# Optimization experiments

Hardware: AMD Instinct MI355X
Metric: run time of the kernel (lower is better)

## Reference

```python
import jax, jax.numpy as jnp
import numpy as np

EPS = 1e-5
DIM = 1024
HEADS = 8
DIM_HEAD = 64
INNER = HEADS * DIM_HEAD  # 512


def layernorm(x, g, b):
    mu = jnp.mean(x, axis=-1, keepdims=True)
    var = jnp.var(x, axis=-1, keepdims=True)
    return (x - mu) * jax.lax.rsqrt(var + EPS) * g + b


def setup_inputs() -> dict:
    key = jax.random.key(0)
    ks = jax.random.split(key, 5)
    b, t, n, m = 4, 4, 2048, 64
    x = jax.random.normal(ks[0], (b, t, n, DIM), dtype=jnp.float32)
    latents = jax.random.normal(ks[1], (b, t, m, DIM), dtype=jnp.float32)
    Wq = jax.random.normal(ks[2], (DIM, INNER), dtype=jnp.float32) * (DIM ** -0.5)
    Wkv = jax.random.normal(ks[3], (DIM, 2 * INNER), dtype=jnp.float32) * (DIM ** -0.5)
    Wo = jax.random.normal(ks[4], (INNER, DIM), dtype=jnp.float32) * (INNER ** -0.5)
    return {
        "x": x, "latents": latents,
        "g_x": jnp.ones((DIM,), jnp.float32), "b_x": jnp.zeros((DIM,), jnp.float32),
        "g_l": jnp.ones((DIM,), jnp.float32), "b_l": jnp.zeros((DIM,), jnp.float32),
        "Wq": Wq, "Wkv": Wkv, "Wo": Wo,
    }


def reference(x, latents, g_x, b_x, g_l, b_l, Wq, Wkv, Wo):
    b, t, n, d = x.shape
    m = latents.shape[2]
    h, dh = HEADS, DIM_HEAD
    scale = dh ** -0.5

    xn = layernorm(x, g_x, b_x)              # (b,t,n,d)
    ln = layernorm(latents, g_l, b_l)        # (b,t,m,d)

    q = jnp.einsum('btmd,de->btme', ln, Wq)  # (b,t,m,inner)
    kv_in = jnp.concatenate([xn, ln], axis=-2)           # (b,t,n+m,d)
    kv = jnp.einsum('btjd,de->btje', kv_in, Wkv)         # (b,t,n+m,2*inner)
    k, v = jnp.split(kv, 2, axis=-1)

    q = q.reshape(b, t, m, h, dh) * scale
    k = k.reshape(b, t, n + m, h, dh)
    v = v.reshape(b, t, n + m, h, dh)

    sim = jnp.einsum('btihd,btjhd->bhtij', q, k)         # (b,h,t,m,n+m)
    sim = sim - jax.lax.stop_gradient(jnp.max(sim, axis=-1, keepdims=True))
    attn = jax.nn.softmax(sim, axis=-1)
    out = jnp.einsum('bhtij,btjhd->btihd', attn, v)      # (b,t,m,h,dh)
    out = out.reshape(b, t, m, h * dh)
    return jnp.einsum('btme,ed->btmd', out, Wo)          # (b,t,m,d)
```

## Files before the change

### kernel.cpp

```cpp
#include <hip/hip_runtime.h>
#include <cstdint>
#include <cstddef>

typedef __attribute__((ext_vector_type(8))) short short8;
typedef __attribute__((ext_vector_type(4))) short short4v;
typedef __attribute__((ext_vector_type(4))) float f32x4;

__device__ __forceinline__ short f2bf(float f) {
    union { float f; unsigned u; } c; c.f = f;
    unsigned r = c.u + 0x7fffu + ((c.u >> 16) & 1u);
    return (short)(r >> 16);
}

__device__ __forceinline__ void gl2lds16(const void* g, void* l) {
    __builtin_amdgcn_global_load_lds(
        (const __attribute__((address_space(1))) void*)g,
        (__attribute__((address_space(3))) void*)l, 16, 0, 0);
}

__global__ __launch_bounds__(256) void wconv_all(
    const float* __restrict__ Wq, const float* __restrict__ Wkv, const float* __restrict__ Wo,
    short* __restrict__ WqT, short* __restrict__ WkvT, short* __restrict__ WoT)
{
    __shared__ float t[32][33];
    const int id = blockIdx.x;
    const float* S; short* D; int K, N, kt, nt; float scale = 1.0f;
    if (id < 1024)      { S = Wkv; D = WkvT; K = 1024; N = 1024; kt = (id >> 5) * 32;          nt = (id & 31) * 32; }
    else if (id < 1536) { S = Wq;  D = WqT;  K = 1024; N = 512;  kt = ((id - 1024) >> 4) * 32; nt = ((id - 1024) & 15) * 32; scale = 0.125f; }
    else                { S = Wo;  D = WoT;  K = 512;  N = 1024; kt = ((id - 1536) >> 5) * 32; nt = ((id - 1536) & 31) * 32; }
    const int x = threadIdx.x & 31, y4 = (threadIdx.x >> 5) * 4;
    for (int i = 0; i < 4; i++)
        t[y4 + i][x] = S[(size_t)(kt + y4 + i) * N + nt + x];
    __syncthreads();
    for (int i = 0; i < 4; i++)
        D[(size_t)(nt + y4 + i) * K + kt + x] = f2bf(t[x][y4 + i] * scale);
}

__global__ __launch_bounds__(256) void ln_kernel(
    const float* __restrict__ x, const float* __restrict__ lat,
    const float* __restrict__ gx, const float* __restrict__ bx,
    const float* __restrict__ gl, const float* __restrict__ bl,
    short* __restrict__ Aout, short* __restrict__ Lq)
{
    const int wave = threadIdx.x >> 6, lane = threadIdx.x & 63;
    const int r = blockIdx.x * 4 + wave;
    const float *src, *g, *b; size_t drow; short* dst2 = nullptr;
    if (r < 32768) {
        int bt = r >> 11, i = r & 2047;
        src = x + (size_t)r * 1024; g = gx; b = bx;
        drow = (size_t)bt * 2112 + i;
    } else {
        int idx = r - 32768;
        int bt = idx >> 6, i = idx & 63;
        src = lat + (size_t)idx * 1024; g = gl; b = bl;
        drow = (size_t)bt * 2112 + 2048 + i;
        dst2 = Lq + (size_t)idx * 1024;
    }
    float4 v[4];
    for (int j = 0; j < 4; j++) v[j] = ((const float4*)src)[lane + 64 * j];
    float s = 0.f, s2 = 0.f;
    for (int j = 0; j < 4; j++) {
        s  += v[j].x + v[j].y + v[j].z + v[j].w;
        s2 += v[j].x * v[j].x + v[j].y * v[j].y + v[j].z * v[j].z + v[j].w * v[j].w;
    }
    for (int off = 32; off >= 1; off >>= 1) { s += __shfl_xor(s, off); s2 += __shfl_xor(s2, off); }
    const float mu   = s * (1.f / 1024.f);
    const float rstd = rsqrtf(s2 * (1.f / 1024.f) - mu * mu + 1e-5f);
    for (int j = 0; j < 4; j++) {
        float4 gv = ((const float4*)g)[lane + 64 * j];
        float4 bv = ((const float4*)b)[lane + 64 * j];
        short4v o;
        o[0] = f2bf((v[j].x - mu) * rstd * gv.x + bv.x);
        o[1] = f2bf((v[j].y - mu) * rstd * gv.y + bv.y);
        o[2] = f2bf((v[j].z - mu) * rstd * gv.z + bv.z);
        o[3] = f2bf((v[j].w - mu) * rstd * gv.w + bv.w);
        *(short4v*)(Aout + drow * 1024 + (size_t)(lane + 64 * j) * 4) = o;
        if (dst2) *(short4v*)(dst2 + (size_t)(lane + 64 * j) * 4) = o;
    }
}

__global__ __launch_bounds__(256) void gemm_kvq(
    const short* __restrict__ A, const short* __restrict__ Bt, short* __restrict__ C,
    const short* __restrict__ Aq, const short* __restrict__ Btq, short* __restrict__ Cq)
{
    __shared__ short As[128 * 32];
    __shared__ short Bs[128 * 32];
    const int tid  = threadIdx.x;
    const int wave = tid >> 6, lane = tid & 63;
    const int col  = lane & 15, quad = lane >> 4;
    const short *pA, *pB; short* pC; int m0, n0, N;
    if (blockIdx.x < 264) {
        pA = A; pB = Bt; pC = C; N = 1024;
        m0 = blockIdx.x * 128; n0 = blockIdx.y * 128;
    } else {
        int extra = (blockIdx.x - 264) * 8 + blockIdx.y;
        pA = Aq; pB = Btq; pC = Cq; N = 512;
        m0 = (extra >> 2) * 128; n0 = (extra & 3) * 128;
    }
    const int K = 1024;
    const int wm = (wave >> 1) * 64, wn = (wave & 1) * 64;
    const int sr = tid >> 2;
    const int sk = (tid & 3) * 8;

    f32x4 acc[4][4];
    for (int i = 0; i < 4; i++) for (int j = 0; j < 4; j++) acc[i][j] = f32x4{0.f, 0.f, 0.f, 0.f};

    const short* Ar0 = pA + (size_t)(m0 + sr)      * K + sk;
    const short* Ar1 = pA + (size_t)(m0 + sr + 64) * K + sk;
    const short* Br0 = pB + (size_t)(n0 + sr)      * K + sk;
    const short* Br1 = pB + (size_t)(n0 + sr + 64) * K + sk;
    short* lA0 = &As[sr * 32 + sk];
    short* lA1 = &As[(sr + 64) * 32 + sk];
    short* lB0 = &Bs[sr * 32 + sk];
    short* lB1 = &Bs[(sr + 64) * 32 + sk];

    for (int k0 = 0; k0 < K; k0 += 32) {
        __syncthreads();
        gl2lds16(Ar0 + k0, lA0);
        gl2lds16(Ar1 + k0, lA1);
        gl2lds16(Br0 + k0, lB0);
        gl2lds16(Br1 + k0, lB1);
        __syncthreads();
        short8 af[4], bf[4];
        for (int mt = 0; mt < 4; mt++) af[mt] = *(const short8*)&As[(wm + mt * 16 + col) * 32 + quad * 8];
        for (int nt = 0; nt < 4; nt++) bf[nt] = *(const short8*)&Bs[(wn + nt * 16 + col) * 32 + quad * 8];
        for (int mt = 0; mt < 4; mt++)
            for (int nt = 0; nt < 4; nt++)
                acc[mt][nt] = __builtin_amdgcn_mfma_f32_16x16x32_bf16(af[mt], bf[nt], acc[mt][nt], 0, 0, 0);
    }
    for (int mt = 0; mt < 4; mt++)
        for (int nt = 0; nt < 4; nt++)
            for (int r = 0; r < 4; r++) {
                int row = m0 + wm + mt * 16 + quad * 4 + r;
                int cc  = n0 + wn + nt * 16 + col;
                pC[(size_t)row * N + cc] = f2bf(acc[mt][nt][r]);
            }
}

template <typename OutT>
__global__ __launch_bounds__(256) void gemm_bt(
    const short* __restrict__ A, const short* __restrict__ Bt,
    OutT* __restrict__ C, int N, int K)
{
    __shared__ short As[128 * 32];
    __shared__ short Bs[128 * 32];
    const int tid  = threadIdx.x;
    const int wave = tid >> 6, lane = tid & 63;
    const int col  = lane & 15, quad = lane >> 4;
    const int m0 = blockIdx.x * 128, n0 = blockIdx.y * 128;
    const int wm = (wave >> 1) * 64, wn = (wave & 1) * 64;
    const int sr = tid >> 2;
    const int sk = (tid & 3) * 8;

    f32x4 acc[4][4];
    for (int i = 0; i < 4; i++) for (int j = 0; j < 4; j++) acc[i][j] = f32x4{0.f, 0.f, 0.f, 0.f};

    const short* Ar0 = A  + (size_t)(m0 + sr)      * K + sk;
    const short* Ar1 = A  + (size_t)(m0 + sr + 64) * K + sk;
    const short* Br0 = Bt + (size_t)(n0 + sr)      * K + sk;
    const short* Br1 = Bt + (size_t)(n0 + sr + 64) * K + sk;
    short* lA0 = &As[sr * 32 + sk];
    short* lA1 = &As[(sr + 64) * 32 + sk];
    short* lB0 = &Bs[sr * 32 + sk];
    short* lB1 = &Bs[(sr + 64) * 32 + sk];

    for (int k0 = 0; k0 < K; k0 += 32) {
        __syncthreads();
        gl2lds16(Ar0 + k0, lA0);
        gl2lds16(Ar1 + k0, lA1);
        gl2lds16(Br0 + k0, lB0);
        gl2lds16(Br1 + k0, lB1);
        __syncthreads();
        short8 af[4], bf[4];
        for (int mt = 0; mt < 4; mt++) af[mt] = *(const short8*)&As[(wm + mt * 16 + col) * 32 + quad * 8];
        for (int nt = 0; nt < 4; nt++) bf[nt] = *(const short8*)&Bs[(wn + nt * 16 + col) * 32 + quad * 8];
        for (int mt = 0; mt < 4; mt++)
            for (int nt = 0; nt < 4; nt++)
                acc[mt][nt] = __builtin_amdgcn_mfma_f32_16x16x32_bf16(af[mt], bf[nt], acc[mt][nt], 0, 0, 0);
    }
    for (int mt = 0; mt < 4; mt++)
        for (int nt = 0; nt < 4; nt++)
            for (int r = 0; r < 4; r++) {
                int row = m0 + wm + mt * 16 + quad * 4 + r;
                int cc  = n0 + wn + nt * 16 + col;
                float v = acc[mt][nt][r];
                if constexpr (sizeof(OutT) == 2) C[(size_t)row * N + cc] = (OutT)f2bf(v);
                else                             C[(size_t)row * N + cc] = v;
            }
}

__global__ __launch_bounds__(256) void transpose_v(const short* __restrict__ KV, short* __restrict__ Vt)
{
    __shared__ short tile[64 * 68];
    const int bth = blockIdx.y, bt = bth >> 3, h = bth & 7;
    const int jt = blockIdx.x * 64;
    const int tid = threadIdx.x;
    for (int it = 0; it < 2; ++it) {
        int s = tid + it * 256;
        int j = s >> 3, dv = (s & 7) * 8;
        short8 v = *(const short8*)(KV + (size_t)(bt * 2112 + jt + j) * 1024 + 512 + h * 64 + dv);
        short4v lo = {v[0], v[1], v[2], v[3]}, hi = {v[4], v[5], v[6], v[7]};
        *(short4v*)&tile[j * 68 + dv]     = lo;
        *(short4v*)&tile[j * 68 + dv + 4] = hi;
    }
    __syncthreads();
    for (int it = 0; it < 2; ++it) {
        int s = tid + it * 256;
        int d = s >> 3, jv = (s & 7) * 8;
        short8 o;
        for (int jj = 0; jj < 8; jj++) o[jj] = tile[(jv + jj) * 68 + d];
        *(short8*)(Vt + (size_t)(bth * 64 + d) * 2112 + jt + jv) = o;
    }
}

__global__ __launch_bounds__(256) void attn_kernel(
    const short* __restrict__ Q,
    const short* __restrict__ KV,
    const short* __restrict__ Vt,
    float* __restrict__ Opart,
    float* __restrict__ Mp,
    float* __restrict__ Lp)
{
    __shared__ __align__(16) short p_lds[4][64 * 72];
    __shared__ float sm[4][64];
    __shared__ float sl[4][64];
    float* oacc = (float*)&p_lds[0][0];

    const int wg = blockIdx.x;
    const int ck = blockIdx.y;
    const int wgc = wg * 4 + ck;
    const int bt = wg >> 3, h = wg & 7;
    const int tid = threadIdx.x;
    const int wave = tid >> 6, lane = tid & 63;
    const int col = lane & 15, quad = lane >> 4;

    short8 qf[4][2];
    for (int mt = 0; mt < 4; mt++)
        for (int ks = 0; ks < 2; ks++)
            qf[mt][ks] = *(const short8*)(Q + (size_t)(bt * 64 + mt * 16 + col) * 512
                                            + h * 64 + ks * 32 + quad * 8);

    float m_run[4][4], l_run[4][4];
    f32x4 o_acc[4][4];
    for (int mt = 0; mt < 4; mt++)
        for (int r = 0; r < 4; r++) { m_run[mt][r] = -__builtin_inff(); l_run[mt][r] = 0.f; }
    for (int mt = 0; mt < 4; mt++)
        for (int dt = 0; dt < 4; dt++) o_acc[mt][dt] = f32x4{0.f, 0.f, 0.f, 0.f};

    short* pl = p_lds[wave];

    for (int jb = ck * 4 + wave; jb < 33; jb += 16) {
        f32x4 s[4][4];
        for (int mt = 0; mt < 4; mt++) for (int nt = 0; nt < 4; nt++) s[mt][nt] = f32x4{0.f, 0.f, 0.f, 0.f};
        for (int nt = 0; nt < 4; nt++) {
            const int j = jb * 64 + nt * 16 + col;
            const short* kp = KV + (size_t)(bt * 2112 + j) * 1024 + h * 64 + quad * 8;
            short8 k0 = *(const short8*)kp;
            short8 k1 = *(const short8*)(kp + 32);
            for (int mt = 0; mt < 4; mt++) {
                s[mt][nt] = __builtin_amdgcn_mfma_f32_16x16x32_bf16(qf[mt][0], k0, s[mt][nt], 0, 0, 0);
                s[mt][nt] = __builtin_amdgcn_mfma_f32_16x16x32_bf16(qf[mt][1], k1, s[mt][nt], 0, 0, 0);
            }
        }
        for (int mt = 0; mt < 4; mt++)
            for (int r = 0; r < 4; r++) {
                float mx = fmaxf(fmaxf(s[mt][0][r], s[mt][1][r]), fmaxf(s[mt][2][r], s[mt][3][r]));
                for (int off = 8; off >= 1; off >>= 1) mx = fmaxf(mx, __shfl_xor(mx, off));
                float mnew = fmaxf(m_run[mt][r], mx);
                float alpha = __expf(m_run[mt][r] - mnew);
                float rs = 0.f;
                for (int nt = 0; nt < 4; nt++) {
                    float p = __expf(s[mt][nt][r] - mnew);
                    s[mt][nt][r] = p;
                    rs += p;
                }
                for (int off = 8; off >= 1; off >>= 1) rs += __shfl_xor(rs, off);
                m_run[mt][r] = mnew;
                l_run[mt][r] = l_run[mt][r] * alpha + rs;
                for (int dt = 0; dt < 4; dt++) o_acc[mt][dt][r] *= alpha;
            }
        for (int mt = 0; mt < 4; mt++)
            for (int nt = 0; nt < 4; nt++)
                for (int r = 0; r < 4; r++)
                    pl[(mt * 16 + quad * 4 + r) * 72 + nt * 16 + col] = f2bf(s[mt][nt][r]);
        for (int ks = 0; ks < 2; ks++) {
            short8 vf[4];
            for (int dt = 0; dt < 4; dt++)
                vf[dt] = *(const short8*)(Vt + (size_t)(wg * 64 + dt * 16 + col) * 2112
                                             + jb * 64 + ks * 32 + quad * 8);
            for (int mt = 0; mt < 4; mt++) {
                short8 pf = *(const short8*)(pl + (mt * 16 + col) * 72 + ks * 32 + quad * 8);
                for (int dt = 0; dt < 4; dt++)
                    o_acc[mt][dt] = __builtin_amdgcn_mfma_f32_16x16x32_bf16(pf, vf[dt], o_acc[mt][dt], 0, 0, 0);
            }
        }
    }

    if (col == 0)
        for (int mt = 0; mt < 4; mt++)
            for (int r = 0; r < 4; r++) {
                int row = mt * 16 + quad * 4 + r;
                sm[wave][row] = m_run[mt][r];
                sl[wave][row] = l_run[mt][r];
            }
    __syncthreads();
    for (int mt = 0; mt < 4; mt++)
        for (int r = 0; r < 4; r++) {
            int row = mt * 16 + quad * 4 + r;
            float M = fmaxf(fmaxf(sm[0][row], sm[1][row]), fmaxf(sm[2][row], sm[3][row]));
            float L = sl[0][row] * __expf(sm[0][row] - M) + sl[1][row] * __expf(sm[1][row] - M)
                    + sl[2][row] * __expf(sm[2][row] - M) + sl[3][row] * __expf(sm[3][row] - M);
            if (wave == 0 && col == 0) { Mp[wgc * 64 + row] = M; Lp[wgc * 64 + row] = L; }
            float sc = __expf(m_run[mt][r] - M);
            for (int dt = 0; dt < 4; dt++) o_acc[mt][dt][r] *= sc;
        }
    for (int i = tid; i < 64 * 64; i += 256) oacc[i] = 0.f;
    __syncthreads();
    for (int w = 0; w < 4; w++) {
        if (wave == w)
            for (int mt = 0; mt < 4; mt++)
                for (int dt = 0; dt < 4; dt++)
                    for (int r = 0; r < 4; r++)
                        oacc[(mt * 16 + quad * 4 + r) * 64 + dt * 16 + col] += o_acc[mt][dt][r];
        __syncthreads();
    }
    for (int i = tid; i < 64 * 64; i += 256)
        Opart[(size_t)wgc * 4096 + i] = oacc[i];
}

__global__ __launch_bounds__(256) void attn_merge(
    const float* __restrict__ Opart, const float* __restrict__ Mp,
    const float* __restrict__ Lp, short* __restrict__ AttO)
{
    int idx = blockIdx.x * 256 + threadIdx.x;
    int wg = idx >> 12, rd = idx & 4095, row = rd >> 6, d = rd & 63;
    float M = -__builtin_inff();
    for (int c = 0; c < 4; c++) M = fmaxf(M, Mp[(wg * 4 + c) * 64 + row]);
    float L = 0.f, O = 0.f;
    for (int c = 0; c < 4; c++) {
        float e = __expf(Mp[(wg * 4 + c) * 64 + row] - M);
        L += e * Lp[(wg * 4 + c) * 64 + row];
        O += e * Opart[(size_t)(wg * 4 + c) * 4096 + rd];
    }
    int bt = wg >> 3, h = wg & 7;
    AttO[(size_t)(bt * 64 + row) * 512 + h * 64 + d] = f2bf(O / L);
}

extern "C" void kernel_launch(void* const* d_in, const int* in_sizes, int n_in,
                              void* d_out, int out_size, void* d_ws, size_t ws_size,
                              hipStream_t stream)
{
    const float* x   = (const float*)d_in[0];
    const float* lat = (const float*)d_in[1];
    const float* g_x = (const float*)d_in[2];
    const float* b_x = (const float*)d_in[3];
    const float* g_l = (const float*)d_in[4];
    const float* b_l = (const float*)d_in[5];
    const float* Wq  = (const float*)d_in[6];
    const float* Wkv = (const float*)d_in[7];
    const float* Wo  = (const float*)d_in[8];
    float* out = (float*)d_out;

    char* ws = (char*)d_ws;
    size_t off = 0;
    auto alloc = [&](size_t bytes) { char* p = ws + off; off += (bytes + 255) & ~(size_t)255; return p; };
    short* A_kvin = (short*)alloc(33792ull * 1024 * 2);
    short* Lq     = (short*)alloc(1024ull * 1024 * 2);
    short* WkvT   = (short*)alloc(1024ull * 1024 * 2);
    short* WqT    = (short*)alloc(512ull * 1024 * 2);
    short* WoT    = (short*)alloc(1024ull * 512 * 2);
    short* KVb    = (short*)alloc(33792ull * 1024 * 2);
    short* Qb     = (short*)alloc(1024ull * 512 * 2);
    short* AttO   = (short*)alloc(1024ull * 512 * 2);
    short* Vt    = A_kvin;
    char*  sc2   = (char*)A_kvin + 36ull * 1024 * 1024;
    float* Opart = (float*)sc2;
    float* Mp    = (float*)(sc2 + 8388608);
    float* Lp    = (float*)(sc2 + 8388608 + 131072);

    wconv_all<<<2048, 256, 0, stream>>>(Wq, Wkv, Wo, WqT, WkvT, WoT);
    ln_kernel<<<8448, 256, 0, stream>>>(x, lat, g_x, b_x, g_l, b_l, A_kvin, Lq);
    gemm_kvq<<<dim3(268, 8), 256, 0, stream>>>(A_kvin, WkvT, KVb, Lq, WqT, Qb);
    transpose_v<<<dim3(33, 128), 256, 0, stream>>>(KVb, Vt);
    attn_kernel<<<dim3(128, 4), 256, 0, stream>>>(Qb, KVb, Vt, Opart, Mp, Lp);
    attn_merge<<<2048, 256, 0, stream>>>(Opart, Mp, Lp, AttO);
    gemm_bt<float><<<dim3(8, 8), 256, 0, stream>>>(AttO, WoT, out, 1024, 512);
}
```

Before: 388.3 us.

## Fuse V transpose into KV GEMM epilogue, merge prep kernels, deepen K step

The KV projection epilogue now writes K to a separate compact buffer and writes V directly in the transposed per-head layout. This removes the standalone transpose_v kernel and its extra read and write of V. The weight conversion and layernorm kernels are merged into one launch, and both GEMMs now stage 64 of K per barrier pair using two LDS buffers, halving the number of syncs. The risks are the uncoalesced short4 scattered stores in the V epilogue and the larger LDS footprint per block.

```diff
diff --git a/kernel.cpp b/kernel.cpp
--- a/kernel.cpp
+++ b/kernel.cpp
@@ -18,83 +18,83 @@
         (__attribute__((address_space(3))) void*)l, 16, 0, 0);
 }
 
-__global__ __launch_bounds__(256) void wconv_all(
-    const float* __restrict__ Wq, const float* __restrict__ Wkv, const float* __restrict__ Wo,
-    short* __restrict__ WqT, short* __restrict__ WkvT, short* __restrict__ WoT)
-{
-    __shared__ float t[32][33];
-    const int id = blockIdx.x;
-    const float* S; short* D; int K, N, kt, nt; float scale = 1.0f;
-    if (id < 1024)      { S = Wkv; D = WkvT; K = 1024; N = 1024; kt = (id >> 5) * 32;          nt = (id & 31) * 32; }
-    else if (id < 1536) { S = Wq;  D = WqT;  K = 1024; N = 512;  kt = ((id - 1024) >> 4) * 32; nt = ((id - 1024) & 15) * 32; scale = 0.125f; }
-    else                { S = Wo;  D = WoT;  K = 512;  N = 1024; kt = ((id - 1536) >> 5) * 32; nt = ((id - 1536) & 31) * 32; }
-    const int x = threadIdx.x & 31, y4 = (threadIdx.x >> 5) * 4;
-    for (int i = 0; i < 4; i++)
-        t[y4 + i][x] = S[(size_t)(kt + y4 + i) * N + nt + x];
-    __syncthreads();
-    for (int i = 0; i < 4; i++)
-        D[(size_t)(nt + y4 + i) * K + kt + x] = f2bf(t[x][y4 + i] * scale);
-}
-
-__global__ __launch_bounds__(256) void ln_kernel(
+__global__ __launch_bounds__(256) void prep_kernel(
     const float* __restrict__ x, const float* __restrict__ lat,
     const float* __restrict__ gx, const float* __restrict__ bx,
     const float* __restrict__ gl, const float* __restrict__ bl,
-    short* __restrict__ Aout, short* __restrict__ Lq)
-{
-    const int wave = threadIdx.x >> 6, lane = threadIdx.x & 63;
-    const int r = blockIdx.x * 4 + wave;
-    const float *src, *g, *b; size_t drow; short* dst2 = nullptr;
-    if (r < 32768) {
-        int bt = r >> 11, i = r & 2047;
-        src = x + (size_t)r * 1024; g = gx; b = bx;
-        drow = (size_t)bt * 2112 + i;
+    short* __restrict__ Aout, short* __restrict__ Lq,
+    const float* __restrict__ Wq, const float* __restrict__ Wkv, const float* __restrict__ Wo,
+    short* __restrict__ WqT, short* __restrict__ WkvT, short* __restrict__ WoT)
+{
+    __shared__ float t[32][33];
+    if (blockIdx.x < 8448) {
+        const int wave = threadIdx.x >> 6, lane = threadIdx.x & 63;
+        const int r = blockIdx.x * 4 + wave;
+        const float *src, *g, *b; size_t drow; short* dst2 = nullptr;
+        if (r < 32768) {
+            int bt = r >> 11, i = r & 2047;
+            src = x + (size_t)r * 1024; g = gx; b = bx;
+            drow = (size_t)bt * 2112 + i;
+        } else {
+            int idx = r - 32768;
+            int bt = idx >> 6, i = idx & 63;
+            src = lat + (size_t)idx * 1024; g = gl; b = bl;
+            drow = (size_t)bt * 2112 + 2048 + i;
+            dst2 = Lq + (size_t)idx * 1024;
+        }
+        float4 v[4];
+        for (int j = 0; j < 4; j++) v[j] = ((const float4*)src)[lane + 64 * j];
+        float s = 0.f, s2 = 0.f;
+        for (int j = 0; j < 4; j++) {
+            s  += v[j].x + v[j].y + v[j].z + v[j].w;
+            s2 += v[j].x * v[j].x + v[j].y * v[j].y + v[j].z * v[j].z + v[j].w * v[j].w;
+        }
+        for (int off = 32; off >= 1; off >>= 1) { s += __shfl_xor(s, off); s2 += __shfl_xor(s2, off); }
+        const float mu   = s * (1.f / 1024.f);
+        const float rstd = rsqrtf(s2 * (1.f / 1024.f) - mu * mu + 1e-5f);
+        for (int j = 0; j < 4; j++) {
+            float4 gv = ((const float4*)g)[lane + 64 * j];
+            float4 bv = ((const float4*)b)[lane + 64 * j];
+            short4v o;
+            o[0] = f2bf((v[j].x - mu) * rstd * gv.x + bv.x);
+            o[1] = f2bf((v[j].y - mu) * rstd * gv.y + bv.y);
+            o[2] = f2bf((v[j].z - mu) * rstd * gv.z + bv.z);
+            o[3] = f2bf((v[j].w - mu) * rstd * gv.w + bv.w);
+            *(short4v*)(Aout + drow * 1024 + (size_t)(lane + 64 * j) * 4) = o;
+            if (dst2) *(short4v*)(dst2 + (size_t)(lane + 64 * j) * 4) = o;
+        }
     } else {
-        int idx = r - 32768;
-        int bt = idx >> 6, i = idx & 63;
-        src = lat + (size_t)idx * 1024; g = gl; b = bl;
-        drow = (size_t)bt * 2112 + 2048 + i;
-        dst2 = Lq + (size_t)idx * 1024;
-    }
-    float4 v[4];
-    for (int j = 0; j < 4; j++) v[j] = ((const float4*)src)[lane + 64 * j];
-    float s = 0.f, s2 = 0.f;
-    for (int j = 0; j < 4; j++) {
-        s  += v[j].x + v[j].y + v[j].z + v[j].w;
-        s2 += v[j].x * v[j].x + v[j].y * v[j].y + v[j].z * v[j].z + v[j].w * v[j].w;
-    }
-    for (int off = 32; off >= 1; off >>= 1) { s += __shfl_xor(s, off); s2 += __shfl_xor(s2, off); }
-    const float mu   = s * (1.f / 1024.f);
-    const float rstd = rsqrtf(s2 * (1.f / 1024.f) - mu * mu + 1e-5f);
-    for (int j = 0; j < 4; j++) {
-        float4 gv = ((const float4*)g)[lane + 64 * j];
-        float4 bv = ((const float4*)b)[lane + 64 * j];
-        short4v o;
-        o[0] = f2bf((v[j].x - mu) * rstd * gv.x + bv.x);
-        o[1] = f2bf((v[j].y - mu) * rstd * gv.y + bv.y);
-        o[2] = f2bf((v[j].z - mu) * rstd * gv.z + bv.z);
-        o[3] = f2bf((v[j].w - mu) * rstd * gv.w + bv.w);
-        *(short4v*)(Aout + drow * 1024 + (size_t)(lane + 64 * j) * 4) = o;
-        if (dst2) *(short4v*)(dst2 + (size_t)(lane + 64 * j) * 4) = o;
+        const int id = blockIdx.x - 8448;
+        const float* S; short* D; int K, N, kt, nt; float scale = 1.0f;
+        if (id < 1024)      { S = Wkv; D = WkvT; K = 1024; N = 1024; kt = (id >> 5) * 32;          nt = (id & 31) * 32; }
+        else if (id < 1536) { S = Wq;  D = WqT;  K = 1024; N = 512;  kt = ((id - 1024) >> 4) * 32; nt = ((id - 1024) & 15) * 32; scale = 0.125f; }
+        else                { S = Wo;  D = WoT;  K = 512;  N = 1024; kt = ((id - 1536) >> 5) * 32; nt = ((id - 1536) & 31) * 32; }
+        const int xx = threadIdx.x & 31, y4 = (threadIdx.x >> 5) * 4;
+        for (int i = 0; i < 4; i++)
+            t[y4 + i][xx] = S[(size_t)(kt + y4 + i) * N + nt + xx];
+        __syncthreads();
+        for (int i = 0; i < 4; i++)
+            D[(size_t)(nt + y4 + i) * K + kt + xx] = f2bf(t[xx][y4 + i] * scale);
     }
 }
 
 __global__ __launch_bounds__(256) void gemm_kvq(
-    const short* __restrict__ A, const short* __restrict__ Bt, short* __restrict__ C,
-    const short* __restrict__ Aq, const short* __restrict__ Btq, short* __restrict__ Cq)
-{
-    __shared__ short As[128 * 32];
-    __shared__ short Bs[128 * 32];
+    const short* __restrict__ A, const short* __restrict__ Bt,
+    short* __restrict__ Kb, short* __restrict__ Vt,
+    const short* __restrict__ Aq, const short* __restrict__ Btq, short* __restrict__ Qb)
+{
+    __shared__ short As0[128 * 32], As1[128 * 32];
+    __shared__ short Bs0[128 * 32], Bs1[128 * 32];
     const int tid  = threadIdx.x;
     const int wave = tid >> 6, lane = tid & 63;
     const int col  = lane & 15, quad = lane >> 4;
-    const short *pA, *pB; short* pC; int m0, n0, N;
+    const short *pA, *pB; int m0, n0, kvmode;
     if (blockIdx.x < 264) {
-        pA = A; pB = Bt; pC = C; N = 1024;
+        pA = A; pB = Bt; kvmode = 1;
         m0 = blockIdx.x * 128; n0 = blockIdx.y * 128;
     } else {
         int extra = (blockIdx.x - 264) * 8 + blockIdx.y;
-        pA = Aq; pB = Btq; pC = Cq; N = 512;
+        pA = Aq; pB = Btq; kvmode = 0;
         m0 = (extra >> 2) * 128; n0 = (extra & 3) * 128;
     }
     const int K = 1024;
@@ -109,113 +109,123 @@
     const short* Ar1 = pA + (size_t)(m0 + sr + 64) * K + sk;
     const short* Br0 = pB + (size_t)(n0 + sr)      * K + sk;
     const short* Br1 = pB + (size_t)(n0 + sr + 64) * K + sk;
-    short* lA0 = &As[sr * 32 + sk];
-    short* lA1 = &As[(sr + 64) * 32 + sk];
-    short* lB0 = &Bs[sr * 32 + sk];
-    short* lB1 = &Bs[(sr + 64) * 32 + sk];
-
-    for (int k0 = 0; k0 < K; k0 += 32) {
-        __syncthreads();
-        gl2lds16(Ar0 + k0, lA0);
-        gl2lds16(Ar1 + k0, lA1);
-        gl2lds16(Br0 + k0, lB0);
-        gl2lds16(Br1 + k0, lB1);
-        __syncthreads();
-        short8 af[4], bf[4];
-        for (int mt = 0; mt < 4; mt++) af[mt] = *(const short8*)&As[(wm + mt * 16 + col) * 32 + quad * 8];
-        for (int nt = 0; nt < 4; nt++) bf[nt] = *(const short8*)&Bs[(wn + nt * 16 + col) * 32 + quad * 8];
+    short* lA0 = &As0[sr * 32 + sk];  short* lA1 = &As0[(sr + 64) * 32 + sk];
+    short* lA2 = &As1[sr * 32 + sk];  short* lA3 = &As1[(sr + 64) * 32 + sk];
+    short* lB0 = &Bs0[sr * 32 + sk];  short* lB1 = &Bs0[(sr + 64) * 32 + sk];
+    short* lB2 = &Bs1[sr * 32 + sk];  short* lB3 = &Bs1[(sr + 64) * 32 + sk];
+
+    for (int k0 = 0; k0 < K; k0 += 64) {
+        __syncthreads();
+        gl2lds16(Ar0 + k0, lA0);      gl2lds16(Ar1 + k0, lA1);
+        gl2lds16(Ar0 + k0 + 32, lA2); gl2lds16(Ar1 + k0 + 32, lA3);
+        gl2lds16(Br0 + k0, lB0);      gl2lds16(Br1 + k0, lB1);
+        gl2lds16(Br0 + k0 + 32, lB2); gl2lds16(Br1 + k0 + 32, lB3);
+        __syncthreads();
+        {
+            short8 af[4], bf[4];
+            for (int mt = 0; mt < 4; mt++) af[mt] = *(const short8*)&As0[(wm + mt * 16 + col) * 32 + quad * 8];
+            for (int nt = 0; nt < 4; nt++) bf[nt] = *(const short8*)&Bs0[(wn + nt * 16 + col) * 32 + quad * 8];
+            for (int mt = 0; mt < 4; mt++)
+                for (int nt = 0; nt < 4; nt++)
+                    acc[mt][nt] = __builtin_amdgcn_mfma_f32_16x16x32_bf16(af[mt], bf[nt], acc[mt][nt], 0, 0, 0);
+        }
+        {
+            short8 af[4], bf[4];
+            for (int mt = 0; mt < 4; mt++) af[mt] = *(const short8*)&As1[(wm + mt * 16 + col) * 32 + quad * 8];
+            for (int nt = 0; nt < 4; nt++) bf[nt] = *(const short8*)&Bs1[(wn + nt * 16 + col) * 32 + quad * 8];
+            for (int mt = 0; mt < 4; mt++)
+                for (int nt = 0; nt < 4; nt++)
+                    acc[mt][nt] = __builtin_amdgcn_mfma_f32_16x16x32_bf16(af[mt], bf[nt], acc[mt][nt], 0, 0, 0);
+        }
+    }
+    if (kvmode) {
+        for (int mt = 0; mt < 4; mt++)
+            for (int nt = 0; nt < 4; nt++) {
+                int ng = n0 + wn + nt * 16 + col;
+                int base_m = m0 + wm + mt * 16 + quad * 4;
+                if (ng < 512) {
+                    for (int r = 0; r < 4; r++)
+                        Kb[(size_t)(base_m + r) * 512 + ng] = f2bf(acc[mt][nt][r]);
+                } else {
+                    int nv = ng - 512, h = nv >> 6, d = nv & 63;
+                    int bt = base_m / 2112, j = base_m - bt * 2112;
+                    short4v pk;
+                    for (int r = 0; r < 4; r++) pk[r] = f2bf(acc[mt][nt][r]);
+                    *(short4v*)&Vt[(size_t)((bt * 8 + h) * 64 + d) * 2112 + j] = pk;
+                }
+            }
+    } else {
         for (int mt = 0; mt < 4; mt++)
             for (int nt = 0; nt < 4; nt++)
-                acc[mt][nt] = __builtin_amdgcn_mfma_f32_16x16x32_bf16(af[mt], bf[nt], acc[mt][nt], 0, 0, 0);
+                for (int r = 0; r < 4; r++) {
+                    int row = m0 + wm + mt * 16 + quad * 4 + r;
+                    int cc  = n0 + wn + nt * 16 + col;
+                    Qb[(size_t)row * 512 + cc] = f2bf(acc[mt][nt][r]);
+                }
+    }
+}
+
+__global__ __launch_bounds__(256) void gemm_out(
+    const short* __restrict__ A, const short* __restrict__ Bt, float* __restrict__ C)
+{
+    __shared__ short As0[128 * 32], As1[128 * 32];
+    __shared__ short Bs0[128 * 32], Bs1[128 * 32];
+    const int tid  = threadIdx.x;
+    const int wave = tid >> 6, lane = tid & 63;
+    const int col  = lane & 15, quad = lane >> 4;
+    const int m0 = blockIdx.x * 128, n0 = blockIdx.y * 128;
+    const int K = 512, N = 1024;
+    const int wm = (wave >> 1) * 64, wn = (wave & 1) * 64;
+    const int sr = tid >> 2, sk = (tid & 3) * 8;
+
+    f32x4 acc[4][4];
+    for (int i = 0; i < 4; i++) for (int j = 0; j < 4; j++) acc[i][j] = f32x4{0.f, 0.f, 0.f, 0.f};
+
+    const short* Ar0 = A  + (size_t)(m0 + sr)      * K + sk;
+    const short* Ar1 = A  + (size_t)(m0 + sr + 64) * K + sk;
+    const short* Br0 = Bt + (size_t)(n0 + sr)      * K + sk;
+    const short* Br1 = Bt + (size_t)(n0 + sr + 64) * K + sk;
+    short* lA0 = &As0[sr * 32 + sk];  short* lA1 = &As0[(sr + 64) * 32 + sk];
+    short* lA2 = &As1[sr * 32 + sk];  short* lA3 = &As1[(sr + 64) * 32 + sk];
+    short* lB0 = &Bs0[sr * 32 + sk];  short* lB1 = &Bs0[(sr + 64) * 32 + sk];
+    short* lB2 = &Bs1[sr * 32 + sk];  short* lB3 = &Bs1[(sr + 64) * 32 + sk];
+
+    for (int k0 = 0; k0 < K; k0 += 64) {
+        __syncthreads();
+        gl2lds16(Ar0 + k0, lA0);      gl2lds16(Ar1 + k0, lA1);
+        gl2lds16(Ar0 + k0 + 32, lA2); gl2lds16(Ar1 + k0 + 32, lA3);
+        gl2lds16(Br0 + k0, lB0);      gl2lds16(Br1 + k0, lB1);
+        gl2lds16(Br0 + k0 + 32, lB2); gl2lds16(Br1 + k0 + 32, lB3);
+        __syncthreads();
+        {
+            short8 af[4], bf[4];
+            for (int mt = 0; mt < 4; mt++) af[mt] = *(const short8*)&As0[(wm + mt * 16 + col) * 32 + quad * 8];
+            for (int nt = 0; nt < 4; nt++) bf[nt] = *(const short8*)&Bs0[(wn + nt * 16 + col) * 32 + quad * 8];
+            for (int mt = 0; mt < 4; mt++)
+                for (int nt = 0; nt < 4; nt++)
+                    acc[mt][nt] = __builtin_amdgcn_mfma_f32_16x16x32_bf16(af[mt], bf[nt], acc[mt][nt], 0, 0, 0);
+        }
+        {
+            short8 af[4], bf[4];
+            for (int mt = 0; mt < 4; mt++) af[mt] = *(const short8*)&As1[(wm + mt * 16 + col) * 32 + quad * 8];
+            for (int nt = 0; nt < 4; nt++) bf[nt] = *(const short8*)&Bs1[(wn + nt * 16 + col) * 32 + quad * 8];
+            for (int mt = 0; mt < 4; mt++)
+                for (int nt = 0; nt < 4; nt++)
+                    acc[mt][nt] = __builtin_amdgcn_mfma_f32_16x16x32_bf16(af[mt], bf[nt], acc[mt][nt], 0, 0, 0);
+        }
     }
     for (int mt = 0; mt < 4; mt++)
         for (int nt = 0; nt < 4; nt++)
             for (int r = 0; r < 4; r++) {
                 int row = m0 + wm + mt * 16 + quad * 4 + r;
                 int cc  = n0 + wn + nt * 16 + col;
-                pC[(size_t)row * N + cc] = f2bf(acc[mt][nt][r]);
-            }
-}
-
-template <typename OutT>
-__global__ __launch_bounds__(256) void gemm_bt(
-    const short* __restrict__ A, const short* __restrict__ Bt,
-    OutT* __restrict__ C, int N, int K)
-{
-    __shared__ short As[128 * 32];
-    __shared__ short Bs[128 * 32];
-    const int tid  = threadIdx.x;
-    const int wave = tid >> 6, lane = tid & 63;
-    const int col  = lane & 15, quad = lane >> 4;
-    const int m0 = blockIdx.x * 128, n0 = blockIdx.y * 128;
-    const int wm = (wave >> 1) * 64, wn = (wave & 1) * 64;
-    const int sr = tid >> 2;
-    const int sk = (tid & 3) * 8;
-
-    f32x4 acc[4][4];
-    for (int i = 0; i < 4; i++) for (int j = 0; j < 4; j++) acc[i][j] = f32x4{0.f, 0.f, 0.f, 0.f};
-
-    const short* Ar0 = A  + (size_t)(m0 + sr)      * K + sk;
-    const short* Ar1 = A  + (size_t)(m0 + sr + 64) * K + sk;
-    const short* Br0 = Bt + (size_t)(n0 + sr)      * K + sk;
-    const short* Br1 = Bt + (size_t)(n0 + sr + 64) * K + sk;
-    short* lA0 = &As[sr * 32 + sk];
-    short* lA1 = &As[(sr + 64) * 32 + sk];
-    short* lB0 = &Bs[sr * 32 + sk];
-    short* lB1 = &Bs[(sr + 64) * 32 + sk];
-
-    for (int k0 = 0; k0 < K; k0 += 32) {
-        __syncthreads();
-        gl2lds16(Ar0 + k0, lA0);
-        gl2lds16(Ar1 + k0, lA1);
-        gl2lds16(Br0 + k0, lB0);
-        gl2lds16(Br1 + k0, lB1);
-        __syncthreads();
-        short8 af[4], bf[4];
-        for (int mt = 0; mt < 4; mt++) af[mt] = *(const short8*)&As[(wm + mt * 16 + col) * 32 + quad * 8];
-        for (int nt = 0; nt < 4; nt++) bf[nt] = *(const short8*)&Bs[(wn + nt * 16 + col) * 32 + quad * 8];
-        for (int mt = 0; mt < 4; mt++)
-            for (int nt = 0; nt < 4; nt++)
-                acc[mt][nt] = __builtin_amdgcn_mfma_f32_16x16x32_bf16(af[mt], bf[nt], acc[mt][nt], 0, 0, 0);
-    }
-    for (int mt = 0; mt < 4; mt++)
-        for (int nt = 0; nt < 4; nt++)
-            for (int r = 0; r < 4; r++) {
-                int row = m0 + wm + mt * 16 + quad * 4 + r;
-                int cc  = n0 + wn + nt * 16 + col;
-                float v = acc[mt][nt][r];
-                if constexpr (sizeof(OutT) == 2) C[(size_t)row * N + cc] = (OutT)f2bf(v);
-                else                             C[(size_t)row * N + cc] = v;
-            }
-}
-
-__global__ __launch_bounds__(256) void transpose_v(const short* __restrict__ KV, short* __restrict__ Vt)
-{
-    __shared__ short tile[64 * 68];
-    const int bth = blockIdx.y, bt = bth >> 3, h = bth & 7;
-    const int jt = blockIdx.x * 64;
-    const int tid = threadIdx.x;
-    for (int it = 0; it < 2; ++it) {
-        int s = tid + it * 256;
-        int j = s >> 3, dv = (s & 7) * 8;
-        short8 v = *(const short8*)(KV + (size_t)(bt * 2112 + jt + j) * 1024 + 512 + h * 64 + dv);
-        short4v lo = {v[0], v[1], v[2], v[3]}, hi = {v[4], v[5], v[6], v[7]};
-        *(short4v*)&tile[j * 68 + dv]     = lo;
-        *(short4v*)&tile[j * 68 + dv + 4] = hi;
-    }
-    __syncthreads();
-    for (int it = 0; it < 2; ++it) {
-        int s = tid + it * 256;
-        int d = s >> 3, jv = (s & 7) * 8;
-        short8 o;
-        for (int jj = 0; jj < 8; jj++) o[jj] = tile[(jv + jj) * 68 + d];
-        *(short8*)(Vt + (size_t)(bth * 64 + d) * 2112 + jt + jv) = o;
-    }
+                C[(size_t)row * N + cc] = acc[mt][nt][r];
+            }
 }
 
 __global__ __launch_bounds__(256) void attn_kernel(
     const short* __restrict__ Q,
-    const short* __restrict__ KV,
+    const short* __restrict__ Kb,
     const short* __restrict__ Vt,
     float* __restrict__ Opart,
     float* __restrict__ Mp,
@@ -254,7 +264,7 @@
         for (int mt = 0; mt < 4; mt++) for (int nt = 0; nt < 4; nt++) s[mt][nt] = f32x4{0.f, 0.f, 0.f, 0.f};
         for (int nt = 0; nt < 4; nt++) {
             const int j = jb * 64 + nt * 16 + col;
-            const short* kp = KV + (size_t)(bt * 2112 + j) * 1024 + h * 64 + quad * 8;
+            const short* kp = Kb + (size_t)(bt * 2112 + j) * 512 + h * 64 + quad * 8;
             short8 k0 = *(const short8*)kp;
             short8 k1 = *(const short8*)(kp + 32);
             for (int mt = 0; mt < 4; mt++) {
@@ -369,20 +379,18 @@
     short* WkvT   = (short*)alloc(1024ull * 1024 * 2);
     short* WqT    = (short*)alloc(512ull * 1024 * 2);
     short* WoT    = (short*)alloc(1024ull * 512 * 2);
-    short* KVb    = (short*)alloc(33792ull * 1024 * 2);
+    short* Kb     = (short*)alloc(33792ull * 512 * 2);
+    short* Vt     = (short*)alloc(33792ull * 512 * 2);
     short* Qb     = (short*)alloc(1024ull * 512 * 2);
     short* AttO   = (short*)alloc(1024ull * 512 * 2);
-    short* Vt    = A_kvin;
-    char*  sc2   = (char*)A_kvin + 36ull * 1024 * 1024;
-    float* Opart = (float*)sc2;
-    float* Mp    = (float*)(sc2 + 8388608);
-    float* Lp    = (float*)(sc2 + 8388608 + 131072);
-
-    wconv_all<<<2048, 256, 0, stream>>>(Wq, Wkv, Wo, WqT, WkvT, WoT);
-    ln_kernel<<<8448, 256, 0, stream>>>(x, lat, g_x, b_x, g_l, b_l, A_kvin, Lq);
-    gemm_kvq<<<dim3(268, 8), 256, 0, stream>>>(A_kvin, WkvT, KVb, Lq, WqT, Qb);
-    transpose_v<<<dim3(33, 128), 256, 0, stream>>>(KVb, Vt);
-    attn_kernel<<<dim3(128, 4), 256, 0, stream>>>(Qb, KVb, Vt, Opart, Mp, Lp);
+    float* Opart  = (float*)alloc(512ull * 4096 * 4);
+    float* Mp     = (float*)alloc(512ull * 64 * 4);
+    float* Lp     = (float*)alloc(512ull * 64 * 4);
+
+    prep_kernel<<<10496, 256, 0, stream>>>(x, lat, g_x, b_x, g_l, b_l, A_kvin, Lq,
+                                           Wq, Wkv, Wo, WqT, WkvT, WoT);
+    gemm_kvq<<<dim3(268, 8), 256, 0, stream>>>(A_kvin, WkvT, Kb, Vt, Lq, WqT, Qb);
+    attn_kernel<<<dim3(128, 4), 256, 0, stream>>>(Qb, Kb, Vt, Opart, Mp, Lp);
     attn_merge<<<2048, 256, 0, stream>>>(Opart, Mp, Lp, AttO);
-    gemm_bt<float><<<dim3(8, 8), 256, 0, stream>>>(AttO, WoT, out, 1024, 512);
-}
+    gemm_out<<<dim3(8, 8), 256, 0, stream>>>(AttO, WoT, out);
+}
```

Result: no change. 385.1 us (-0.8%).
